# Kernel optimization log

Hardware: AMD Instinct MI355X
Metric: run time of the kernel (lower is better)

## Reference

```python
import jax, jax.numpy as jnp
import numpy as np

HEADS = 8
DIM_HEAD = 32
SCALE = DIM_HEAD ** (-0.5)


def setup_inputs() -> dict:
    key = jax.random.key(0)
    k1, k2, k3, k4 = jax.random.split(key, 4)
    x = jax.random.normal(k1, (16, 256, 64, 64), dtype=jnp.float32)
    # conv 1x1 weights stored as [out_ch, in_ch]
    w_qkv = jax.random.normal(k2, (3 * HEADS * DIM_HEAD, 256), dtype=jnp.float32) * 0.05
    w_out = jax.random.normal(k3, (256, HEADS * DIM_HEAD), dtype=jnp.float32) * 0.05
    b_out = jax.random.normal(k4, (256,), dtype=jnp.float32) * 0.05
    return {"x": x, "w_qkv": w_qkv, "w_out": w_out, "b_out": b_out}


def reference(x, w_qkv, w_out, b_out):
    b, c, h, w = x.shape
    n = h * w
    # 1x1 conv (no bias) == channel matmul
    qkv = jnp.einsum('bchw,oc->bohw', x, w_qkv)            # [b, 3*H*D, h, w]
    qkv = qkv.reshape(b, 3, HEADS, DIM_HEAD, n)            # chunk then 'b (h c) xy'
    q, k, v = qkv[:, 0], qkv[:, 1], qkv[:, 2]              # [b, H, D, n]
    q = jax.nn.softmax(q, axis=-2) * SCALE                 # softmax over channel dim d
    k = jax.nn.softmax(k, axis=-1)                         # softmax over spatial n
    context = jnp.einsum('bhdn,bhen->bhde', k, v)          # [b, H, D, D]
    out = jnp.einsum('bhde,bhdn->bhen', context, q)        # [b, H, D, n]
    out = out.reshape(b, HEADS * DIM_HEAD, h, w)
    # 1x1 conv with bias
    return jnp.einsum('bchw,oc->bohw', out, w_out) + b_out[None, :, None, None]
```

## Files before the change

kernel.cpp:

```cpp
#include <hip/hip_runtime.h>
#include <cstddef>
#include <cstdint>

#define NN 4096
#define CIN 256
#define CQKV 768
#define NBATCH 16
#define QSCALE 0.17677669529663687f

typedef short s16x8 __attribute__((ext_vector_type(8)));
typedef float f32x4 __attribute__((ext_vector_type(4)));

__device__ __forceinline__ float bf2f(unsigned short u) {
    unsigned int x = ((unsigned int)u) << 16;
    return __builtin_bit_cast(float, x);
}
__device__ __forceinline__ unsigned short f2bf(float f) {
    unsigned int u = __builtin_bit_cast(unsigned int, f);
    return (unsigned short)((u + 0x7fffu + ((u >> 16) & 1u)) >> 16);
}
__device__ __forceinline__ void glds16(const void* gsrc, void* lds) {
    __builtin_amdgcn_global_load_lds(
        (const __attribute__((address_space(1))) unsigned int*)gsrc,
        (__attribute__((address_space(3))) unsigned int*)lds,
        16, 0, 0);
}

__global__ __launch_bounds__(256)
void prep(const float* __restrict__ x, unsigned short* __restrict__ xT,
          const float* __restrict__ w, unsigned short* __restrict__ wb)
{
    const int t = threadIdx.x;
    if (blockIdx.z < NBATCH) {
        const int b = blockIdx.z;
        const int n0 = blockIdx.x * 64, c0 = blockIdx.y * 64;
        __shared__ float xs[64][65];
        const float* xb = x + (size_t)b * CIN * NN;
#pragma unroll
        for (int p = 0; p < 4; ++p) {
            const int row = p * 16 + (t >> 4);
            const int col = (t & 15) * 4;
            const float4 v = *reinterpret_cast<const float4*>(
                &xb[(size_t)(c0 + row) * NN + n0 + col]);
            xs[col + 0][row] = v.x; xs[col + 1][row] = v.y;
            xs[col + 2][row] = v.z; xs[col + 3][row] = v.w;
        }
        __syncthreads();
        const int n = t >> 2, cch = (t & 3) * 16;
        unsigned short arr[16];
#pragma unroll
        for (int e = 0; e < 16; ++e) arr[e] = f2bf(xs[n][cch + e]);
        unsigned short* dst = xT + ((size_t)b * NN + n0 + n) * 256 + c0 + cch;
        *reinterpret_cast<s16x8*>(&dst[0]) = *reinterpret_cast<s16x8*>(&arr[0]);
        *reinterpret_cast<s16x8*>(&dst[8]) = *reinterpret_cast<s16x8*>(&arr[8]);
    } else {
        const int bid = blockIdx.y * 64 + blockIdx.x;
        if (bid < CQKV * CIN / 1024) {
            const int i = (bid * 256 + t) * 4;
            const float4 v = *reinterpret_cast<const float4*>(&w[i]);
            unsigned short a[4] = { f2bf(v.x), f2bf(v.y), f2bf(v.z), f2bf(v.w) };
            *reinterpret_cast<ushort2*>(&wb[i])     = *reinterpret_cast<ushort2*>(&a[0]);
            *reinterpret_cast<ushort2*>(&wb[i + 2]) = *reinterpret_cast<ushort2*>(&a[2]);
        }
    }
}

__device__ __forceinline__ void gemm_core64(const unsigned short* __restrict__ Ab,
                                            const unsigned short* __restrict__ Bb,
                                            int m0, int n0, char* smem,
                                            f32x4 (&acc)[4][4])
{
    const int t = threadIdx.x;
    const int lane = t & 63, w = t >> 6;
    const int lr = lane & 15, lq = lane >> 4;
    const int wr = (w >> 1) * 64, wc = (w & 1) * 64;
    const int srow = t >> 3;
    const int schunk = (t & 7) ^ (srow & 7);
    const int wq = w << 10;
    const int xr = lr & 7;

    char* A0 = smem;          char* B0 = smem + 16384;
    char* A1 = smem + 32768;  char* B1 = smem + 49152;

#define STG(bufA, bufB, k0)                                                     \
    { _Pragma("unroll") for (int i = 0; i < 4; ++i)                             \
        glds16(Ab + (size_t)(m0 + i*32 + srow)*256 + (k0) + schunk*8,           \
               (bufA) + i*4096 + wq);                                           \
      _Pragma("unroll") for (int i = 0; i < 4; ++i)                             \
        glds16(Bb + (size_t)(n0 + i*32 + srow)*256 + (k0) + schunk*8,           \
               (bufB) + i*4096 + wq); }

#define CMP(bufA, bufB)                                                         \
    { s16x8 af[4][2], bfr[4][2];                                                \
      _Pragma("unroll") for (int m = 0; m < 4; ++m) {                           \
        const char* rp = (bufA) + (wr + m*16 + lr)*128;                         \
        af[m][0] = *(const s16x8*)(rp + (((0*4 + lq) ^ xr) << 4));              \
        af[m][1] = *(const s16x8*)(rp + (((1*4 + lq) ^ xr) << 4)); }            \
      _Pragma("unroll") for (int n = 0; n < 4; ++n) {                           \
        const char* rp = (bufB) + (wc + n*16 + lr)*128;                         \
        bfr[n][0] = *(const s16x8*)(rp + (((0*4 + lq) ^ xr) << 4));             \
        bfr[n][1] = *(const s16x8*)(rp + (((1*4 + lq) ^ xr) << 4)); }           \
      _Pragma("unroll") for (int m = 0; m < 4; ++m)                             \
      _Pragma("unroll") for (int n = 0; n < 4; ++n) {                           \
        acc[m][n] = __builtin_amdgcn_mfma_f32_16x16x32_bf16(af[m][0], bfr[n][0], acc[m][n], 0, 0, 0); \
        acc[m][n] = __builtin_amdgcn_mfma_f32_16x16x32_bf16(af[m][1], bfr[n][1], acc[m][n], 0, 0, 0); }}

    STG(A0, B0, 0);
    __syncthreads();
    STG(A1, B1, 64);
    CMP(A0, B0);
    __syncthreads();
    STG(A0, B0, 128);
    CMP(A1, B1);
    __syncthreads();
    STG(A1, B1, 192);
    CMP(A0, B0);
    __syncthreads();
    CMP(A1, B1);
#undef STG
#undef CMP
}

__global__ __launch_bounds__(256, 2)
void qkv_fused(const unsigned short* __restrict__ wb,
               const unsigned short* __restrict__ xT,
               unsigned short* __restrict__ qT,
               float* __restrict__ ctx_part,
               float* __restrict__ z_part)
{
    __shared__ __align__(16) char smem[65536];
    const int nt = blockIdx.x;
    const int ty = blockIdx.y;
    const int b  = blockIdx.z;
    const int t = threadIdx.x;
    const int lane = t & 63, w = t >> 6;
    const int lr = lane & 15, lq = lane >> 4;
    const int wr = (w >> 1) * 64, wc = (w & 1) * 64;
    const int n0 = nt * 128;

    if (ty < 2) {
        const int m0 = ty * 128;
        const unsigned short* Bb = xT + (size_t)b * NN * 256;
        f32x4 acc[4][4] = {};
        gemm_core64(wb, Bb, m0, n0, smem, acc);

        __syncthreads();
        unsigned short (*qs)[136] = (unsigned short (*)[136])smem;
#pragma unroll
        for (int n = 0; n < 4; ++n) {
            const int col = wc + n * 16 + lr;
#pragma unroll
            for (int hp = 0; hp < 2; ++hp) {
                float mx = -1e30f;
#pragma unroll
                for (int u = 0; u < 2; ++u)
#pragma unroll
                    for (int r = 0; r < 4; ++r)
                        mx = fmaxf(mx, acc[hp * 2 + u][n][r]);
                mx = fmaxf(mx, __shfl_xor(mx, 16));
                mx = fmaxf(mx, __shfl_xor(mx, 32));
                float er[2][4];
                float s = 0.f;
#pragma unroll
                for (int u = 0; u < 2; ++u)
#pragma unroll
                    for (int r = 0; r < 4; ++r) {
                        er[u][r] = __expf(acc[hp * 2 + u][n][r] - mx);
                        s += er[u][r];
                    }
                s += __shfl_xor(s, 16);
                s += __shfl_xor(s, 32);
                const float inv = QSCALE / s;
#pragma unroll
                for (int u = 0; u < 2; ++u) {
                    ushort4 pk;
                    pk.x = f2bf(er[u][0] * inv);
                    pk.y = f2bf(er[u][1] * inv);
                    pk.z = f2bf(er[u][2] * inv);
                    pk.w = f2bf(er[u][3] * inv);
                    *(ushort4*)&qs[col][wr + (hp * 2 + u) * 16 + lq * 4] = pk;
                }
            }
        }
        __syncthreads();
        const int nl = t >> 1, half = t & 1;
        const unsigned short* src = &qs[nl][half * 64];
        unsigned short* dst = qT + ((size_t)b * NN + n0 + nl) * 256 + m0 + half * 64;
#pragma unroll
        for (int i = 0; i < 8; ++i)
            *(s16x8*)(dst + i * 8) = *(const s16x8*)(src + i * 8);
    } else {
        const int g = ty - 2;
        const unsigned short* An = xT + ((size_t)b * NN + (size_t)n0) * 256;

        f32x4 acc[4][4] = {};
        gemm_core64(An, wb, 0, 256 + g * 128, smem, acc);

        unsigned int ekpk[4][4][2];
        float zl[4] = {0.f, 0.f, 0.f, 0.f};
#pragma unroll
        for (int m = 0; m < 4; ++m)
#pragma unroll
            for (int nn = 0; nn < 4; ++nn) {
                const unsigned short u0 = f2bf(__expf(acc[m][nn][0]));
                const unsigned short u1 = f2bf(__expf(acc[m][nn][1]));
                const unsigned short u2 = f2bf(__expf(acc[m][nn][2]));
                const unsigned short u3 = f2bf(__expf(acc[m][nn][3]));
                zl[nn] += bf2f(u0) + bf2f(u1) + bf2f(u2) + bf2f(u3);
                ekpk[m][nn][0] = (unsigned int)u0 | ((unsigned int)u1 << 16);
                ekpk[m][nn][1] = (unsigned int)u2 | ((unsigned int)u3 << 16);
            }
#pragma unroll
        for (int nn = 0; nn < 4; ++nn) {
            zl[nn] += __shfl_xor(zl[nn], 16);
            zl[nn] += __shfl_xor(zl[nn], 32);
        }
        const float zv = (lq == 0) ? zl[0] : (lq == 1) ? zl[1] : (lq == 2) ? zl[2] : zl[3];
        z_part[((((size_t)(b * 32 + nt)) * 2 + g) * 2 + (w >> 1)) * 128 + wc + lane] = zv;

#pragma unroll
        for (int m = 0; m < 4; ++m)
#pragma unroll
            for (int nn = 0; nn < 4; ++nn) acc[m][nn] = (f32x4){0.f, 0.f, 0.f, 0.f};
        gemm_core64(An, wb, 0, 512 + g * 128, smem, acc);

        __syncthreads();
#pragma unroll
        for (int m = 0; m < 4; ++m)
#pragma unroll
            for (int nn = 0; nn < 4; ++nn) {
                const int col = wc + nn * 16 + lr;
                const int swz = (col & 7) << 4;
                const int rowb = (wr + m * 16 + lq * 4) * 2;
                *(unsigned int*)(smem + ((col * 256 + rowb) ^ swz))       = ekpk[m][nn][0];
                *(unsigned int*)(smem + ((col * 256 + rowb + 4) ^ swz))   = ekpk[m][nn][1];
                const unsigned int vp0 = (unsigned int)f2bf(acc[m][nn][0])
                                       | ((unsigned int)f2bf(acc[m][nn][1]) << 16);
                const unsigned int vp1 = (unsigned int)f2bf(acc[m][nn][2])
                                       | ((unsigned int)f2bf(acc[m][nn][3]) << 16);
                *(unsigned int*)(smem + 32768 + ((col * 256 + rowb) ^ swz))     = vp0;
                *(unsigned int*)(smem + 32768 + ((col * 256 + rowb + 4) ^ swz)) = vp1;
            }
        __syncthreads();

        f32x4 cacc[2][2] = {};
#pragma unroll
        for (int ks = 0; ks < 4; ++ks) {
            s16x8 af[2], bfv[2];
#pragma unroll
            for (int dt = 0; dt < 2; ++dt) {
                const int drow = w * 32 + dt * 16 + lr;
                af[dt] = *(const s16x8*)(smem +
                    ((drow * 256 + ks * 64 + lq * 16) ^ ((drow & 7) << 4)));
            }
#pragma unroll
            for (int et = 0; et < 2; ++et) {
                const int erow = w * 32 + et * 16 + lr;
                bfv[et] = *(const s16x8*)(smem + 32768 +
                    ((erow * 256 + ks * 64 + lq * 16) ^ ((erow & 7) << 4)));
            }
#pragma unroll
            for (int dt = 0; dt < 2; ++dt)
#pragma unroll
                for (int et = 0; et < 2; ++et)
                    cacc[dt][et] = __builtin_amdgcn_mfma_f32_16x16x32_bf16(
                        af[dt], bfv[et], cacc[dt][et], 0, 0, 0);
        }
        float* cp = ctx_part + ((((size_t)(b * 32 + nt)) * 2 + g) * 4 + w) * 1024;
#pragma unroll
        for (int dt = 0; dt < 2; ++dt)
#pragma unroll
            for (int et = 0; et < 2; ++et)
#pragma unroll
                for (int r = 0; r < 4; ++r)
                    cp[(dt * 16 + lq * 4 + r) * 32 + et * 16 + lr] = cacc[dt][et][r];
    }
}

__global__ __launch_bounds__(256)
void make_m(const float* __restrict__ ctx_part, const float* __restrict__ z_part,
            const float* __restrict__ w_out, unsigned short* __restrict__ Mmat)
{
    const int h = blockIdx.x, b = blockIdx.y;
    const int g = h >> 2, hh = h & 3;
    const int t = threadIdx.x;
    __shared__ float ctx[32][33];
    __shared__ float zinv[32];

    for (int c = t; c < 1024; c += 256) {
        float s = 0.f;
#pragma unroll 8
        for (int nt = 0; nt < 32; ++nt)
            s += ctx_part[((((size_t)(b * 32 + nt)) * 2 + g) * 4 + hh) * 1024 + c];
        ctx[c >> 5][c & 31] = s;
    }
    if (t < 32) {
        float z = 0.f;
#pragma unroll 8
        for (int nt = 0; nt < 32; ++nt) {
            const size_t base = (((size_t)(b * 32 + nt)) * 2 + g) * 2;
            z += z_part[(base + 0) * 128 + hh * 32 + t];
            z += z_part[(base + 1) * 128 + hh * 32 + t];
        }
        zinv[t] = 1.f / z;
    }
    __syncthreads();

    const int o = t;
    float wrow[32];
#pragma unroll
    for (int e = 0; e < 32; ++e)
        wrow[e] = w_out[(size_t)o * 256 + h * 32 + e];
#pragma unroll 4
    for (int d = 0; d < 32; ++d) {
        float s = 0.f;
#pragma unroll
        for (int e = 0; e < 32; ++e)
            s = fmaf(wrow[e], ctx[d][e], s);
        Mmat[((size_t)b * 256 + o) * 256 + h * 32 + d] = f2bf(s * zinv[d]);
    }
}

__global__ __launch_bounds__(256, 2)
void gemm_out(const unsigned short* __restrict__ Mmat,
              const unsigned short* __restrict__ qT,
              float* __restrict__ out, const float* __restrict__ bias)
{
    __shared__ __align__(16) char smem[65536];
    const int bz = blockIdx.z;
    const int m0 = blockIdx.y * 128, n0 = blockIdx.x * 128;
    const unsigned short* Ab = Mmat + (size_t)bz * 256 * 256;
    const unsigned short* Bb = qT + (size_t)bz * NN * 256;

    f32x4 acc[4][4] = {};
    gemm_core64(Ab, Bb, m0, n0, smem, acc);

    const int t = threadIdx.x;
    const int lane = t & 63, w = t >> 6;
    const int lr = lane & 15, lq = lane >> 4;
    const int wr = (w >> 1) * 64, wc = (w & 1) * 64;

    __syncthreads();
#pragma unroll
    for (int m = 0; m < 4; ++m)
#pragma unroll
        for (int r = 0; r < 4; ++r) {
            const int row = wr + m * 16 + lq * 4 + r;
            const float bv = bias[m0 + row];
            const int rb = row * 512;
            const int xs = (row & 7) << 4;
#pragma unroll
            for (int n = 0; n < 4; ++n) {
                const int col = wc + n * 16 + lr;
                *(float*)(smem + rb + ((col * 4) ^ xs)) = acc[m][n][r] + bv;
            }
        }
    __syncthreads();

    float* Yb = out + (size_t)bz * CIN * NN;
#pragma unroll
    for (int p = 0; p < 8; ++p) {
        const int row = p * 16 + (t >> 4);
        const int rb = row * 512;
        const int xs = (row & 7) << 4;
        const int cb = (t & 15) * 32;
        const float4 v0 = *(const float4*)(smem + rb + ((cb + 0) ^ xs));
        const float4 v1 = *(const float4*)(smem + rb + ((cb + 16) ^ xs));
        float* dst = Yb + (size_t)(m0 + row) * NN + n0 + (t & 15) * 8;
        *(float4*)dst = v0;
        *(float4*)(dst + 4) = v1;
    }
}

extern "C" void kernel_launch(void* const* d_in, const int* in_sizes, int n_in,
                              void* d_out, int out_size, void* d_ws, size_t ws_size,
                              hipStream_t stream)
{
    const float* x     = (const float*)d_in[0];
    const float* w_qkv = (const float*)d_in[1];
    const float* w_out = (const float*)d_in[2];
    const float* b_out = (const float*)d_in[3];
    float* out = (float*)d_out;

    char* ws = (char*)d_ws;
    size_t off = 0;
    unsigned short* xT  = (unsigned short*)(ws + off);  off += (size_t)NBATCH * NN * CIN * 2;
    unsigned short* qT  = (unsigned short*)(ws + off);  off += (size_t)NBATCH * NN * CIN * 2;
    float* ctx_part     = (float*)(ws + off);           off += (size_t)NBATCH * 32 * 2 * 4 * 1024 * 4;
    float* z_part       = (float*)(ws + off);           off += (size_t)NBATCH * 32 * 2 * 2 * 128 * 4;
    unsigned short* Mmat= (unsigned short*)(ws + off);  off += (size_t)NBATCH * 256 * 256 * 2;
    unsigned short* wb  = (unsigned short*)(ws + off);  off += (size_t)CQKV * CIN * 2;

    prep<<<dim3(NN / 64, CIN / 64, NBATCH + 1), 256, 0, stream>>>(x, xT, w_qkv, wb);

    qkv_fused<<<dim3(32, 4, NBATCH), 256, 0, stream>>>(wb, xT, qT, ctx_part, z_part);

    make_m<<<dim3(8, NBATCH), 256, 0, stream>>>(ctx_part, z_part, w_out, Mmat);

    gemm_out<<<dim3(32, 2, NBATCH), 256, 0, stream>>>(Mmat, qT, out, b_out);
}
```

Baseline: 103.4 us.

## Fuse K and V projections into one asymmetric GEMM with interleaved weights

The prep kernel now reorders the K/V rows of the bf16 weight copy so that each head group's K and V rows sit next to each other. The K/V path of qkv_fused then runs one 128x256 GEMM instead of two sequential 128x128 GEMMs, so the x tile is loaded and staged once rather than twice. The new GEMM uses a triple-buffered global_load_lds pipeline with explicit vmcnt waits and setprio around the MFMA block. The context GEMM is rebuilt to write exp(K) and V through LDS in two passes, one per row half. This raises LDS use to 72KB and accumulator registers to 4x8 tiles, which can reduce occupancy below two blocks per CU.

Result: slower. 109.4 us (+5.8%).

```diff
diff --git a/kernel.cpp b/kernel.cpp
--- a/kernel.cpp
+++ b/kernel.cpp
@@ -28,7 +28,7 @@
 
 __global__ __launch_bounds__(256)
 void prep(const float* __restrict__ x, unsigned short* __restrict__ xT,
-          const float* __restrict__ w, unsigned short* __restrict__ wb)
+          const float* __restrict__ w, unsigned short* __restrict__ wb2)
 {
     const int t = threadIdx.x;
     if (blockIdx.z < NBATCH) {
@@ -57,10 +57,21 @@
         const int bid = blockIdx.y * 64 + blockIdx.x;
         if (bid < CQKV * CIN / 1024) {
             const int i = (bid * 256 + t) * 4;
-            const float4 v = *reinterpret_cast<const float4*>(&w[i]);
+            const int row = i >> 8, col = i & 255;
+            int orow;
+            if (row < 256) orow = row;
+            else {
+                const int g = (row - 256) >> 8;
+                const int within = (row - 256) & 255;
+                const int half = within >> 7;
+                const int idx = within & 127;
+                orow = 256 + half * 256 + g * 128 + idx;
+            }
+            const float4 v = *reinterpret_cast<const float4*>(
+                &w[(size_t)orow * 256 + col]);
             unsigned short a[4] = { f2bf(v.x), f2bf(v.y), f2bf(v.z), f2bf(v.w) };
-            *reinterpret_cast<ushort2*>(&wb[i])     = *reinterpret_cast<ushort2*>(&a[0]);
-            *reinterpret_cast<ushort2*>(&wb[i + 2]) = *reinterpret_cast<ushort2*>(&a[2]);
+            *reinterpret_cast<ushort2*>(&wb2[i])     = *reinterpret_cast<ushort2*>(&a[0]);
+            *reinterpret_cast<ushort2*>(&wb2[i + 2]) = *reinterpret_cast<ushort2*>(&a[2]);
         }
     }
 }
@@ -121,14 +132,76 @@
 #undef CMP
 }
 
+template<int MF, int NF>
+__device__ __forceinline__ void gemm_asym(const unsigned short* __restrict__ Ab,
+                                          const unsigned short* __restrict__ Bb,
+                                          char* __restrict__ smem,
+                                          f32x4 (&acc)[MF][NF])
+{
+    constexpr int AW = MF / 2;
+    constexpr int BW = NF / 2;
+    constexpr int ASTG = MF * 2048;
+    constexpr int BSTG = NF * 2048;
+    const int t = threadIdx.x;
+    const int lane = t & 63, w = t >> 6;
+    const int lr = lane & 15, lq = lane >> 4;
+    const int wr = (w >> 1) * (MF * 16), wc = (w & 1) * (NF * 16);
+    char* Abuf = smem;
+    char* Bbuf = smem + 3 * ASTG;
+
+#define STG_H(h)                                                               \
+  { char* ab = Abuf + ((h) % 3) * ASTG;                                        \
+    char* bb = Bbuf + ((h) % 3) * BSTG;                                        \
+    _Pragma("unroll") for (int j = 0; j < AW; ++j) {                           \
+        const int ch = (w * AW + j) * 64 + lane;                               \
+        const int row = ch >> 2, c = (ch & 3) ^ ((row >> 1) & 3);              \
+        glds16(Ab + (size_t)row * 256 + (h) * 32 + c * 8,                      \
+               ab + (w * AW + j) * 1024); }                                    \
+    _Pragma("unroll") for (int j = 0; j < BW; ++j) {                           \
+        const int ch = (w * BW + j) * 64 + lane;                               \
+        const int row = ch >> 2, c = (ch & 3) ^ ((row >> 1) & 3);              \
+        glds16(Bb + (size_t)row * 256 + (h) * 32 + c * 8,                      \
+               bb + (w * BW + j) * 1024); } }
+
+#define CMP_H(h)                                                               \
+  { char* ab = Abuf + ((h) % 3) * ASTG;                                        \
+    char* bb = Bbuf + ((h) % 3) * BSTG;                                        \
+    s16x8 af[MF], bfr[NF];                                                     \
+    _Pragma("unroll") for (int m = 0; m < MF; ++m) {                           \
+        const int row = wr + m * 16 + lr;                                      \
+        af[m] = *(const s16x8*)(ab + row * 64 + ((lq ^ ((row >> 1) & 3)) << 4)); } \
+    _Pragma("unroll") for (int nn = 0; nn < NF; ++nn) {                        \
+        const int col = wc + nn * 16 + lr;                                     \
+        bfr[nn] = *(const s16x8*)(bb + col * 64 + ((lq ^ ((col >> 1) & 3)) << 4)); } \
+    __builtin_amdgcn_s_setprio(1);                                             \
+    _Pragma("unroll") for (int m = 0; m < MF; ++m)                             \
+    _Pragma("unroll") for (int nn = 0; nn < NF; ++nn)                          \
+        acc[m][nn] = __builtin_amdgcn_mfma_f32_16x16x32_bf16(af[m], bfr[nn],   \
+                                                             acc[m][nn], 0, 0, 0); \
+    __builtin_amdgcn_s_setprio(0); }
+
+    STG_H(0); STG_H(1);
+#pragma unroll
+    for (int i = 0; i < 8; ++i) {
+        if (i < 7) asm volatile("s_waitcnt vmcnt(6)" ::: "memory");
+        else       asm volatile("s_waitcnt vmcnt(0)" ::: "memory");
+        __builtin_amdgcn_s_barrier();
+        __builtin_amdgcn_sched_barrier(0);
+        if (i < 6) STG_H(i + 2);
+        CMP_H(i);
+    }
+#undef STG_H
+#undef CMP_H
+}
+
 __global__ __launch_bounds__(256, 2)
-void qkv_fused(const unsigned short* __restrict__ wb,
+void qkv_fused(const unsigned short* __restrict__ wb2,
                const unsigned short* __restrict__ xT,
                unsigned short* __restrict__ qT,
                float* __restrict__ ctx_part,
                float* __restrict__ z_part)
 {
-    __shared__ __align__(16) char smem[65536];
+    __shared__ __align__(16) char smem[73728];
     const int nt = blockIdx.x;
     const int ty = blockIdx.y;
     const int b  = blockIdx.z;
@@ -137,12 +210,13 @@
     const int lr = lane & 15, lq = lane >> 4;
     const int wr = (w >> 1) * 64, wc = (w & 1) * 64;
     const int n0 = nt * 128;
+    const unsigned short* xslab = xT + ((size_t)b * NN + n0) * 256;
 
     if (ty < 2) {
         const int m0 = ty * 128;
         const unsigned short* Bb = xT + (size_t)b * NN * 256;
         f32x4 acc[4][4] = {};
-        gemm_core64(wb, Bb, m0, n0, smem, acc);
+        gemm_core64(wb2, Bb, m0, n0, smem, acc);
 
         __syncthreads();
         unsigned short (*qs)[136] = (unsigned short (*)[136])smem;
@@ -191,80 +265,78 @@
             *(s16x8*)(dst + i * 8) = *(const s16x8*)(src + i * 8);
     } else {
         const int g = ty - 2;
-        const unsigned short* An = xT + ((size_t)b * NN + (size_t)n0) * 256;
-
-        f32x4 acc[4][4] = {};
-        gemm_core64(An, wb, 0, 256 + g * 128, smem, acc);
-
-        unsigned int ekpk[4][4][2];
-        float zl[4] = {0.f, 0.f, 0.f, 0.f};
-#pragma unroll
-        for (int m = 0; m < 4; ++m)
-#pragma unroll
-            for (int nn = 0; nn < 4; ++nn) {
-                const unsigned short u0 = f2bf(__expf(acc[m][nn][0]));
-                const unsigned short u1 = f2bf(__expf(acc[m][nn][1]));
-                const unsigned short u2 = f2bf(__expf(acc[m][nn][2]));
-                const unsigned short u3 = f2bf(__expf(acc[m][nn][3]));
-                zl[nn] += bf2f(u0) + bf2f(u1) + bf2f(u2) + bf2f(u3);
-                ekpk[m][nn][0] = (unsigned int)u0 | ((unsigned int)u1 << 16);
-                ekpk[m][nn][1] = (unsigned int)u2 | ((unsigned int)u3 << 16);
-            }
-#pragma unroll
-        for (int nn = 0; nn < 4; ++nn) {
-            zl[nn] += __shfl_xor(zl[nn], 16);
-            zl[nn] += __shfl_xor(zl[nn], 32);
-        }
-        const float zv = (lq == 0) ? zl[0] : (lq == 1) ? zl[1] : (lq == 2) ? zl[2] : zl[3];
-        z_part[((((size_t)(b * 32 + nt)) * 2 + g) * 2 + (w >> 1)) * 128 + wc + lane] = zv;
-
-#pragma unroll
-        for (int m = 0; m < 4; ++m)
-#pragma unroll
-            for (int nn = 0; nn < 4; ++nn) acc[m][nn] = (f32x4){0.f, 0.f, 0.f, 0.f};
-        gemm_core64(An, wb, 0, 512 + g * 128, smem, acc);
+        f32x4 acc[4][8] = {};
+        gemm_asym<4, 8>(xslab, wb2 + (size_t)(256 + g * 256) * 256, smem, acc);
+
+        if ((w & 1) == 0) {
+            float zl[8];
+#pragma unroll
+            for (int nn = 0; nn < 8; ++nn) zl[nn] = 0.f;
+#pragma unroll
+            for (int m = 0; m < 4; ++m)
+#pragma unroll
+                for (int nn = 0; nn < 8; ++nn)
+#pragma unroll
+                    for (int r = 0; r < 4; ++r) {
+                        const float e = bf2f(f2bf(__expf(acc[m][nn][r])));
+                        acc[m][nn][r] = e;
+                        zl[nn] += e;
+                    }
+#pragma unroll
+            for (int nn = 0; nn < 8; ++nn) {
+                zl[nn] += __shfl_xor(zl[nn], 16);
+                zl[nn] += __shfl_xor(zl[nn], 32);
+            }
+            float* zp = z_part + ((((size_t)(b * 32 + nt)) * 2 + g) * 2 + (w >> 1)) * 128;
+            zp[lane]      = zl[lq];
+            zp[64 + lane] = zl[4 + lq];
+        }
 
         __syncthreads();
-#pragma unroll
-        for (int m = 0; m < 4; ++m)
-#pragma unroll
-            for (int nn = 0; nn < 4; ++nn) {
-                const int col = wc + nn * 16 + lr;
-                const int swz = (col & 7) << 4;
-                const int rowb = (wr + m * 16 + lq * 4) * 2;
-                *(unsigned int*)(smem + ((col * 256 + rowb) ^ swz))       = ekpk[m][nn][0];
-                *(unsigned int*)(smem + ((col * 256 + rowb + 4) ^ swz))   = ekpk[m][nn][1];
-                const unsigned int vp0 = (unsigned int)f2bf(acc[m][nn][0])
-                                       | ((unsigned int)f2bf(acc[m][nn][1]) << 16);
-                const unsigned int vp1 = (unsigned int)f2bf(acc[m][nn][2])
-                                       | ((unsigned int)f2bf(acc[m][nn][3]) << 16);
-                *(unsigned int*)(smem + 32768 + ((col * 256 + rowb) ^ swz))     = vp0;
-                *(unsigned int*)(smem + 32768 + ((col * 256 + rowb + 4) ^ swz)) = vp1;
-            }
-        __syncthreads();
-
         f32x4 cacc[2][2] = {};
 #pragma unroll
-        for (int ks = 0; ks < 4; ++ks) {
-            s16x8 af[2], bfv[2];
-#pragma unroll
-            for (int dt = 0; dt < 2; ++dt) {
-                const int drow = w * 32 + dt * 16 + lr;
-                af[dt] = *(const s16x8*)(smem +
-                    ((drow * 256 + ks * 64 + lq * 16) ^ ((drow & 7) << 4)));
-            }
-#pragma unroll
-            for (int et = 0; et < 2; ++et) {
-                const int erow = w * 32 + et * 16 + lr;
-                bfv[et] = *(const s16x8*)(smem + 32768 +
-                    ((erow * 256 + ks * 64 + lq * 16) ^ ((erow & 7) << 4)));
-            }
-#pragma unroll
-            for (int dt = 0; dt < 2; ++dt)
-#pragma unroll
-                for (int et = 0; et < 2; ++et)
-                    cacc[dt][et] = __builtin_amdgcn_mfma_f32_16x16x32_bf16(
-                        af[dt], bfv[et], cacc[dt][et], 0, 0, 0);
+        for (int p = 0; p < 2; ++p) {
+            if ((w >> 1) == p) {
+                char* base = (w & 1) ? (smem + 16384) : smem;
+#pragma unroll
+                for (int m = 0; m < 4; ++m)
+#pragma unroll
+                    for (int nn = 0; nn < 8; ++nn) {
+                        const int col = nn * 16 + lr;
+                        const int swz = (col & 7) << 4;
+                        const int rowb = (m * 16 + lq * 4) * 2;
+                        const unsigned int p0 = (unsigned int)f2bf(acc[m][nn][0])
+                            | ((unsigned int)f2bf(acc[m][nn][1]) << 16);
+                        const unsigned int p1 = (unsigned int)f2bf(acc[m][nn][2])
+                            | ((unsigned int)f2bf(acc[m][nn][3]) << 16);
+                        *(unsigned int*)(base + ((col * 128 + rowb) ^ swz))     = p0;
+                        *(unsigned int*)(base + ((col * 128 + rowb + 4) ^ swz)) = p1;
+                    }
+            }
+            __syncthreads();
+#pragma unroll
+            for (int ks2 = 0; ks2 < 2; ++ks2) {
+                s16x8 afk[2], bfv[2];
+#pragma unroll
+                for (int dt = 0; dt < 2; ++dt) {
+                    const int drow = w * 32 + dt * 16 + lr;
+                    afk[dt] = *(const s16x8*)(smem + drow * 128 +
+                        ((((ks2 * 4 + lq) ^ (drow & 7))) << 4));
+                }
+#pragma unroll
+                for (int et = 0; et < 2; ++et) {
+                    const int erow = w * 32 + et * 16 + lr;
+                    bfv[et] = *(const s16x8*)(smem + 16384 + erow * 128 +
+                        ((((ks2 * 4 + lq) ^ (erow & 7))) << 4));
+                }
+#pragma unroll
+                for (int dt = 0; dt < 2; ++dt)
+#pragma unroll
+                    for (int et = 0; et < 2; ++et)
+                        cacc[dt][et] = __builtin_amdgcn_mfma_f32_16x16x32_bf16(
+                            afk[dt], bfv[et], cacc[dt][et], 0, 0, 0);
+            }
+            __syncthreads();
         }
         float* cp = ctx_part + ((((size_t)(b * 32 + nt)) * 2 + g) * 4 + w) * 1024;
 #pragma unroll
@@ -389,11 +461,11 @@
     float* ctx_part     = (float*)(ws + off);           off += (size_t)NBATCH * 32 * 2 * 4 * 1024 * 4;
     float* z_part       = (float*)(ws + off);           off += (size_t)NBATCH * 32 * 2 * 2 * 128 * 4;
     unsigned short* Mmat= (unsigned short*)(ws + off);  off += (size_t)NBATCH * 256 * 256 * 2;
-    unsigned short* wb  = (unsigned short*)(ws + off);  off += (size_t)CQKV * CIN * 2;
-
-    prep<<<dim3(NN / 64, CIN / 64, NBATCH + 1), 256, 0, stream>>>(x, xT, w_qkv, wb);
-
-    qkv_fused<<<dim3(32, 4, NBATCH), 256, 0, stream>>>(wb, xT, qT, ctx_part, z_part);
+    unsigned short* wb2 = (unsigned short*)(ws + off);  off += (size_t)CQKV * CIN * 2;
+
+    prep<<<dim3(NN / 64, CIN / 64, NBATCH + 1), 256, 0, stream>>>(x, xT, w_qkv, wb2);
+
+    qkv_fused<<<dim3(32, 4, NBATCH), 256, 0, stream>>>(wb2, xT, qT, ctx_part, z_part);
 
     make_m<<<dim3(8, NBATCH), 256, 0, stream>>>(ctx_part, z_part, w_out, Mmat);
 
```
